# Kernel optimization log

Measured on AMD Instinct MI355X. Metric: run time of the kernel, lower is better.

The kernel has to match this reference:

```python
import jax, jax.numpy as jnp
import numpy as np

N_EMBD = 1024
N_HEAD = 16
HEAD_SIZE = N_EMBD // N_HEAD
BLOCK_SIZE = 2048
B, T = 2, 2048
EPS = 1e-5


def _layernorm(x, g, b):
    mu = jnp.mean(x, axis=-1, keepdims=True)
    var = jnp.mean(jnp.square(x - mu), axis=-1, keepdims=True)
    return (x - mu) * jax.lax.rsqrt(var + EPS) * g + b


def setup_inputs() -> dict:
    key = jax.random.key(0)
    ks = jax.random.split(key, 12)
    s = 0.02
    x = jax.random.normal(ks[0], (B, T, N_EMBD), dtype=jnp.float32)
    wq = jax.random.normal(ks[1], (N_HEAD, N_EMBD, HEAD_SIZE), jnp.float32) * s
    wk = jax.random.normal(ks[2], (N_HEAD, N_EMBD, HEAD_SIZE), jnp.float32) * s
    wv = jax.random.normal(ks[3], (N_HEAD, N_EMBD, HEAD_SIZE), jnp.float32) * s
    w_proj = jax.random.normal(ks[4], (N_EMBD, N_EMBD), jnp.float32) * s
    b_proj = jnp.zeros((N_EMBD,), jnp.float32)
    w1 = jax.random.normal(ks[5], (N_EMBD, 4 * N_EMBD), jnp.float32) * s
    b1 = jnp.zeros((4 * N_EMBD,), jnp.float32)
    w2 = jax.random.normal(ks[6], (4 * N_EMBD, N_EMBD), jnp.float32) * s
    b2 = jnp.zeros((N_EMBD,), jnp.float32)
    g1 = jnp.ones((N_EMBD,), jnp.float32)
    be1 = jnp.zeros((N_EMBD,), jnp.float32)
    g2 = jnp.ones((N_EMBD,), jnp.float32)
    be2 = jnp.zeros((N_EMBD,), jnp.float32)
    return dict(x=x, wq=wq, wk=wk, wv=wv, w_proj=w_proj, b_proj=b_proj,
                w1=w1, b1=b1, w2=w2, b2=b2, g1=g1, be1=be1, g2=g2, be2=be2)


def reference(x, wq, wk, wv, w_proj, b_proj, w1, b1, w2, b2, g1, be1, g2, be2):
    # --- self-attention with pre-LN ---
    h = _layernorm(x, g1, be1)
    q = jnp.einsum('btc,hcd->bhtd', h, wq)
    k = jnp.einsum('btc,hcd->bhtd', h, wk)
    v = jnp.einsum('btc,hcd->bhtd', h, wv)
    scores = jnp.einsum('bhtd,bhsd->bhts', q, k) / np.sqrt(HEAD_SIZE).astype(np.float32)
    causal = jnp.tril(jnp.ones((T, T), dtype=bool))
    scores = jnp.where(causal, scores, -jnp.inf)
    weights = jax.nn.softmax(scores, axis=-1)
    attn = jnp.einsum('bhts,bhsd->bhtd', weights, v)  # (B,H,T,D)
    attn = attn.transpose(0, 2, 1, 3).reshape(B, T, N_EMBD)  # concat heads
    sa = attn @ w_proj + b_proj
    x = x + sa
    # --- feed-forward with pre-LN ---
    h2 = _layernorm(x, g2, be2)
    ff = jax.nn.relu(h2 @ w1 + b1) @ w2 + b2
    return x + ff
```

## Files before the change

### kernel.cpp

```cpp
#include <hip/hip_runtime.h>
#include <hip/hip_bf16.h>
#include <cstdint>


typedef unsigned short u16;
typedef unsigned int u32;
typedef __attribute__((ext_vector_type(8))) __bf16 bf16x8;
typedef __attribute__((ext_vector_type(4))) float f32x4;

__device__ __forceinline__ u16 f2b(float f) {
    return __builtin_bit_cast(unsigned short, __float2bfloat16(f));
}

__device__ __forceinline__ f32x4 mfma16(bf16x8 a, bf16x8 b, f32x4 c) {
    return __builtin_amdgcn_mfma_f32_16x16x32_bf16(a, b, c, 0, 0, 0);
}

__device__ __forceinline__ void load_lds16(const u16* g, u16* l) {
    __builtin_amdgcn_global_load_lds(
        (const __attribute__((address_space(1))) unsigned int*)g,
        (__attribute__((address_space(3))) unsigned int*)l, 16, 0, 0);
}

__global__ __launch_bounds__(256) void transpose_all(
    const float* __restrict__ wq, const float* __restrict__ wk,
    const float* __restrict__ wv, const float* __restrict__ wp,
    const float* __restrict__ w1, const float* __restrict__ w2,
    u16* __restrict__ wqkvt, u16* __restrict__ wpt,
    u16* __restrict__ w1t, u16* __restrict__ w2t)
{
    __shared__ float tile[32][33];
    int id = blockIdx.x;
    const float* src; u16* dst; int R, C, bx, by;
    if (id < 3072) {
        const int m = id >> 10;
        src = (m == 0) ? wq : (m == 1) ? wk : wv;
        dst = wqkvt + m * 1048576u;
        int t = id & 1023;
        const int b = t >> 6; t &= 63;
        R = 1024; C = 64; bx = t & 1; by = t >> 1;
        src += (size_t)b * 65536; dst += (size_t)b * 65536;
    } else if (id < 4096) {
        int t = id - 3072; src = wp; dst = wpt;
        R = 1024; C = 1024; bx = t & 31; by = t >> 5;
    } else if (id < 8192) {
        int t = id - 4096; src = w1; dst = w1t;
        R = 1024; C = 4096; bx = t & 127; by = t >> 7;
    } else {
        int t = id - 8192; src = w2; dst = w2t;
        R = 4096; C = 1024; bx = t & 31; by = t >> 5;
    }
    const int tx = threadIdx.x, ty = threadIdx.y;
    const int c0 = bx * 32, r0 = by * 32;
#pragma unroll
    for (int i = 0; i < 4; ++i) {
        int r = ty * 4 + i;
        tile[r][tx] = src[(size_t)(r0 + r) * C + c0 + tx];
    }
    __syncthreads();
#pragma unroll
    for (int i = 0; i < 4; ++i) {
        int r = ty * 4 + i;
        dst[(size_t)(c0 + r) * R + r0 + tx] = f2b(tile[tx][r]);
    }
}

__global__ __launch_bounds__(256) void ln_kernel(
    const float* __restrict__ x, const float* __restrict__ g,
    const float* __restrict__ be, u16* __restrict__ out)
{
    const int row = blockIdx.x;
    const int tid = threadIdx.x;
    const float* xr = x + (size_t)row * 1024;
    float v[4];
#pragma unroll
    for (int i = 0; i < 4; ++i) v[i] = xr[tid + i * 256];
    float s = v[0] + v[1] + v[2] + v[3];
    float q = v[0]*v[0] + v[1]*v[1] + v[2]*v[2] + v[3]*v[3];
#pragma unroll
    for (int o = 1; o < 64; o <<= 1) {
        s += __shfl_xor(s, o, 64);
        q += __shfl_xor(q, o, 64);
    }
    __shared__ float red[8];
    const int wave = tid >> 6;
    if ((tid & 63) == 0) { red[wave] = s; red[4 + wave] = q; }
    __syncthreads();
    s = red[0] + red[1] + red[2] + red[3];
    q = red[4] + red[5] + red[6] + red[7];
    const float mu = s * (1.0f / 1024.0f);
    const float var = q * (1.0f / 1024.0f) - mu * mu;
    const float rstd = rsqrtf(var + 1e-5f);
#pragma unroll
    for (int i = 0; i < 4; ++i) {
        int idx = tid + i * 256;
        out[(size_t)row * 1024 + idx] = f2b((v[i] - mu) * rstd * g[idx] + be[idx]);
    }
}

template <int EPI, int TM, int TN, int WM, int WN, int BK>
__global__ __launch_bounds__(256, 2) void gemm_bt(
    const u16* __restrict__ A, const u16* __restrict__ Bt,
    int M, int N, int K,
    const float* __restrict__ bias, const float* __restrict__ resid_f,
    u16* __restrict__ out_b, float* __restrict__ out_f)
{
    constexpr int MI = WM / 16, NI = WN / 16;
    constexpr int MWAVES = TM / WM;
    constexpr int SS = BK / 64;
    __shared__ alignas(16) u16 As[TM * BK];
    __shared__ alignas(16) u16 Bs[TN * BK];
    const int tid = threadIdx.x;
    const int wave = tid >> 6, lane = tid & 63;
    const int lr = lane >> 4, lc = lane & 15;
    const int m0 = blockIdx.x * TM, n0 = blockIdx.y * TN;
    const int wm = (wave % MWAVES) * WM, wn = (wave / MWAVES) * WN;

    f32x4 acc[MI][NI];
#pragma unroll
    for (int i = 0; i < MI; ++i)
#pragma unroll
        for (int j = 0; j < NI; ++j) acc[i][j] = (f32x4){0.f, 0.f, 0.f, 0.f};

    const int srow = lane >> 3;
    const int skb = (lane & 7) ^ srow;
    const u16* Agp = A + (size_t)(m0 + wave * 8 + srow) * K + skb * 8;
    const u16* Bgp = Bt + (size_t)(n0 + wave * 8 + srow) * K + skb * 8;
    const int ldst = wave * 512;

    for (int k0 = 0; k0 < K; k0 += BK) {
#pragma unroll
        for (int s = 0; s < SS; ++s) {
#pragma unroll
            for (int i = 0; i < TM / 32; ++i)
                load_lds16(Agp + (size_t)i * 32 * K + k0 + s * 64,
                           As + s * TM * 64 + i * 2048 + ldst);
#pragma unroll
            for (int i = 0; i < TN / 32; ++i)
                load_lds16(Bgp + (size_t)i * 32 * K + k0 + s * 64,
                           Bs + s * TN * 64 + i * 2048 + ldst);
        }
        __syncthreads();
#pragma unroll
        for (int h = 0; h < BK / 32; ++h) {
            const int ss = h >> 1, hh = h & 1;
            const int qh = ((hh * 4 + lr) ^ (lc & 7)) * 8;
            bf16x8 af[MI], bfr[NI];
#pragma unroll
            for (int i = 0; i < MI; ++i)
                af[i] = *(const bf16x8*)&As[ss * TM * 64 + (wm + i * 16 + lc) * 64 + qh];
#pragma unroll
            for (int j = 0; j < NI; ++j)
                bfr[j] = *(const bf16x8*)&Bs[ss * TN * 64 + (wn + j * 16 + lc) * 64 + qh];
#pragma unroll
            for (int i = 0; i < MI; ++i)
#pragma unroll
                for (int j = 0; j < NI; ++j)
                    acc[i][j] = mfma16(af[i], bfr[j], acc[i][j]);
        }
        __syncthreads();
    }

#pragma unroll
    for (int i = 0; i < MI; ++i) {
#pragma unroll
        for (int j = 0; j < NI; ++j) {
#pragma unroll
            for (int r = 0; r < 4; ++r) {
                const int m = m0 + wm + i * 16 + lr * 4 + r;
                const int n = n0 + wn + j * 16 + lc;
                const float v = acc[i][j][r];
                if (EPI == 0) {
                    const int group = n >> 10, nn = n & 1023;
                    const int hh = nn >> 6, dd = nn & 63;
                    const int bb = m >> 11, tt = m & 2047;
                    if (group == 0)
                        out_b[(((size_t)(bb * 16 + hh) * 2048) + tt) * 64 + dd] =
                            f2b(v * 0.18033688f);
                    else if (group == 1)
                        out_b[4194304u + (((size_t)(bb * 16 + hh) * 2048) + tt) * 64 + dd] =
                            f2b(v);
                    else
                        out_b[8388608u + (((size_t)(bb * 16 + hh) * 64) + dd) * 2048 + tt] =
                            f2b(v);
                } else if (EPI == 4) {
                    size_t idx = (size_t)m * N + n;
                    float rv = v + bias[n];
                    out_b[idx] = f2b(rv > 0.f ? rv : 0.f);
                } else {
                    size_t idx = (size_t)m * N + n;
                    out_f[idx] = resid_f[idx] + v + bias[n];
                }
            }
        }
    }
}

__global__ __launch_bounds__(256) void attn_kernel(
    const u16* __restrict__ qb, const u16* __restrict__ kb,
    const u16* __restrict__ vtb, u16* __restrict__ ob)
{
    const int id = blockIdx.x;
    const int xcd = id & 7;
    const int xq = (id >> 3) & 15;
    const int bh = (id >> 7) * 8 + xcd;
    const int b = bh >> 4, h = bh & 15;
    const int tid = threadIdx.x, wave = tid >> 6, lane = tid & 63;
    const int lr = lane >> 4, lc = lane & 15;
    const int qx = lc & 7;
    __shared__ alignas(16) u16 Ks[64 * 64];
    __shared__ alignas(16) u16 Vts[64 * 64];
    __shared__ alignas(16) u16 Ps[4][16 * 64];
    const size_t base = (size_t)bh * (2048 * 64);

    const int srow = lane >> 3;
    const int sdb = (lane & 7) ^ srow;
    const u16* kg0 = kb + base + (size_t)(wave * 16 + srow) * 64 + sdb * 8;
    const u16* vg0 = vtb + base + (size_t)(wave * 16 + srow) * 2048 + sdb * 8;
    u16* KsW = Ks + wave * 1024;
    u16* VsW = Vts + wave * 1024;
    const int q0 = (lr ^ qx) * 8;
    const int q1 = ((4 + lr) ^ qx) * 8;
    const int wsh = lr >> 1, wsub = (lr & 1) * 4;

    for (int half = 0; half < 2; ++half) {
        const int qt = half ? (31 - xq) : xq;
        const int t0 = qt * 64;
        const int trow = t0 + wave * 16 + lc;
        const bf16x8 qf0 = *(const bf16x8*)&qb[base + (size_t)trow * 64 + lr * 8];
        const bf16x8 qf1 = *(const bf16x8*)&qb[base + (size_t)trow * 64 + 32 + lr * 8];
        f32x4 O[4];
        float pls = 0.f;
#pragma unroll
        for (int j = 0; j < 4; ++j) O[j] = (f32x4){0.f, 0.f, 0.f, 0.f};

        for (int c = 0; c <= qt; ++c) {
            const int s0 = c * 64;
            load_lds16(kg0 + (size_t)s0 * 64, KsW);
            load_lds16(kg0 + (size_t)s0 * 64 + 512, KsW + 512);
            load_lds16(vg0 + s0, VsW);
            load_lds16(vg0 + s0 + 8 * 2048, VsW + 512);
            __syncthreads();

            f32x4 st[4];
#pragma unroll
            for (int j = 0; j < 4; ++j) st[j] = (f32x4){0.f, 0.f, 0.f, 0.f};
#pragma unroll
            for (int j = 0; j < 4; ++j) {
                const int row = (j * 16 + lc) * 64;
                bf16x8 k0 = *(const bf16x8*)&Ks[row + q0];
                bf16x8 k1 = *(const bf16x8*)&Ks[row + q1];
                st[j] = mfma16(k0, qf0, st[j]);
                st[j] = mfma16(k1, qf1, st[j]);
            }
#pragma unroll
            for (int j = 0; j < 4; ++j) {
                float pv[4];
#pragma unroll
                for (int r = 0; r < 4; ++r) {
                    float e = __builtin_amdgcn_exp2f(st[j][r]);
                    if (s0 + j * 16 + lr * 4 + r > trow) e = 0.f;
                    pls += e;
                    pv[r] = e;
                }
                uint2 w;
                w.x = (u32)f2b(pv[0]) | ((u32)f2b(pv[1]) << 16);
                w.y = (u32)f2b(pv[2]) | ((u32)f2b(pv[3]) << 16);
                *(uint2*)&Ps[wave][lc * 64 + (((j * 2 + wsh) ^ qx) * 8) + wsub] = w;
            }
            const bf16x8 pf0 = *(const bf16x8*)&Ps[wave][lc * 64 + q0];
            const bf16x8 pf1 = *(const bf16x8*)&Ps[wave][lc * 64 + q1];
#pragma unroll
            for (int j = 0; j < 4; ++j) {
                const int row = (j * 16 + lc) * 64;
                bf16x8 v0 = *(const bf16x8*)&Vts[row + q0];
                bf16x8 v1 = *(const bf16x8*)&Vts[row + q1];
                O[j] = mfma16(pf0, v0, O[j]);
                O[j] = mfma16(pf1, v1, O[j]);
            }
            __syncthreads();
        }

        float l = pls;
        l += __shfl_xor(l, 16, 64);
        l += __shfl_xor(l, 32, 64);
        const float linvT = 1.0f / l;
        float linv[4];
#pragma unroll
        for (int r = 0; r < 4; ++r) linv[r] = __shfl(linvT, lr * 4 + r, 64);
#pragma unroll
        for (int j = 0; j < 4; ++j)
#pragma unroll
            for (int r = 0; r < 4; ++r) {
                const int tr = t0 + wave * 16 + lr * 4 + r;
                ob[((size_t)b * 2048 + tr) * 1024 + h * 64 + j * 16 + lc] =
                    f2b(O[j][r] * linv[r]);
            }
    }
}

extern "C" void kernel_launch(void* const* d_in, const int* in_sizes, int n_in,
                              void* d_out, int out_size, void* d_ws, size_t ws_size,
                              hipStream_t stream)
{
    (void)in_sizes; (void)n_in; (void)out_size; (void)ws_size;
    const float* x   = (const float*)d_in[0];
    const float* wq  = (const float*)d_in[1];
    const float* wk  = (const float*)d_in[2];
    const float* wv  = (const float*)d_in[3];
    const float* wp  = (const float*)d_in[4];
    const float* bp  = (const float*)d_in[5];
    const float* w1  = (const float*)d_in[6];
    const float* b1  = (const float*)d_in[7];
    const float* w2  = (const float*)d_in[8];
    const float* b2  = (const float*)d_in[9];
    const float* g1  = (const float*)d_in[10];
    const float* be1 = (const float*)d_in[11];
    const float* g2  = (const float*)d_in[12];
    const float* be2 = (const float*)d_in[13];
    float* out = (float*)d_out;

    char* ws = (char*)d_ws;
    const size_t MB = 1024ull * 1024;
    u16*   h1    = (u16*)(ws + 0);
    u16*   wqkvt = (u16*)(ws + 8 * MB);
    u16*   wpt   = (u16*)(ws + 14 * MB);
    u16*   w1t   = (u16*)(ws + 16 * MB);
    u16*   w2t   = (u16*)(ws + 24 * MB);
    u16*   qkv   = (u16*)(ws + 32 * MB);
    u16*   attnb = (u16*)(ws + 56 * MB);
    u16*   ff1   = (u16*)(ws + 32 * MB);
    float* x2    = (float*)(ws + 64 * MB);
    u16*   h2    = h1;
    u16*   qb    = qkv;
    u16*   kbf   = qkv + 4194304u;
    u16*   vtb   = qkv + 8388608u;

    transpose_all<<<12288, dim3(32, 8), 0, stream>>>(
        wq, wk, wv, wp, w1, w2, wqkvt, wpt, w1t, w2t);

    ln_kernel<<<4096, 256, 0, stream>>>(x, g1, be1, h1);

    gemm_bt<0, 128, 128, 64, 64, 64><<<dim3(32, 24), 256, 0, stream>>>(
        h1, wqkvt, 4096, 3072, 1024, nullptr, nullptr, qkv, nullptr);

    attn_kernel<<<512, 256, 0, stream>>>(qb, kbf, vtb, attnb);

    gemm_bt<3, 64, 128, 32, 64, 128><<<dim3(64, 8), 256, 0, stream>>>(
        attnb, wpt, 4096, 1024, 1024, bp, x, nullptr, x2);

    ln_kernel<<<4096, 256, 0, stream>>>(x2, g2, be2, h2);

    gemm_bt<4, 128, 128, 64, 64, 64><<<dim3(32, 32), 256, 0, stream>>>(
        h2, w1t, 4096, 4096, 1024, b1, nullptr, ff1, nullptr);

    gemm_bt<5, 64, 128, 32, 64, 128><<<dim3(64, 8), 256, 0, stream>>>(
        ff1, w2t, 4096, 1024, 4096, b2, x2, nullptr, out);
}
```

Before: 319.7 us.

## Process two adjacent query tiles per block to reuse each K/V tile

```diff
diff --git a/kernel.cpp b/kernel.cpp
--- a/kernel.cpp
+++ b/kernel.cpp
@@ -202,7 +202,7 @@
 {
     const int id = blockIdx.x;
     const int xcd = id & 7;
-    const int xq = (id >> 3) & 15;
+    const int qt = 15 - ((id >> 3) & 15);
     const int bh = (id >> 7) * 8 + xcd;
     const int b = bh >> 4, h = bh & 15;
     const int tid = threadIdx.x, wave = tid >> 6, lane = tid & 63;
@@ -223,25 +223,34 @@
     const int q1 = ((4 + lr) ^ qx) * 8;
     const int wsh = lr >> 1, wsub = (lr & 1) * 4;
 
-    for (int half = 0; half < 2; ++half) {
-        const int qt = half ? (31 - xq) : xq;
-        const int t0 = qt * 64;
-        const int trow = t0 + wave * 16 + lc;
-        const bf16x8 qf0 = *(const bf16x8*)&qb[base + (size_t)trow * 64 + lr * 8];
-        const bf16x8 qf1 = *(const bf16x8*)&qb[base + (size_t)trow * 64 + 32 + lr * 8];
-        f32x4 O[4];
-        float pls = 0.f;
-#pragma unroll
-        for (int j = 0; j < 4; ++j) O[j] = (f32x4){0.f, 0.f, 0.f, 0.f};
-
-        for (int c = 0; c <= qt; ++c) {
-            const int s0 = c * 64;
-            load_lds16(kg0 + (size_t)s0 * 64, KsW);
-            load_lds16(kg0 + (size_t)s0 * 64 + 512, KsW + 512);
-            load_lds16(vg0 + s0, VsW);
-            load_lds16(vg0 + s0 + 8 * 2048, VsW + 512);
-            __syncthreads();
-
+    const int t0 = qt * 128;
+    int trow[2];
+    bf16x8 qf[2][2];
+#pragma unroll
+    for (int u = 0; u < 2; ++u) {
+        trow[u] = t0 + u * 64 + wave * 16 + lc;
+        qf[u][0] = *(const bf16x8*)&qb[base + (size_t)trow[u] * 64 + lr * 8];
+        qf[u][1] = *(const bf16x8*)&qb[base + (size_t)trow[u] * 64 + 32 + lr * 8];
+    }
+    f32x4 O[2][4];
+    float pls[2] = {0.f, 0.f};
+#pragma unroll
+    for (int u = 0; u < 2; ++u)
+#pragma unroll
+        for (int j = 0; j < 4; ++j) O[u][j] = (f32x4){0.f, 0.f, 0.f, 0.f};
+
+    const int nch = 2 * qt + 2;
+    for (int c = 0; c < nch; ++c) {
+        const int s0 = c * 64;
+        load_lds16(kg0 + (size_t)s0 * 64, KsW);
+        load_lds16(kg0 + (size_t)s0 * 64 + 512, KsW + 512);
+        load_lds16(vg0 + s0, VsW);
+        load_lds16(vg0 + s0 + 8 * 2048, VsW + 512);
+        __syncthreads();
+
+#pragma unroll
+        for (int u = 0; u < 2; ++u) {
+            if (u == 0 && s0 >= t0 + 64) continue;
             f32x4 st[4];
 #pragma unroll
             for (int j = 0; j < 4; ++j) st[j] = (f32x4){0.f, 0.f, 0.f, 0.f};
@@ -250,8 +259,8 @@
                 const int row = (j * 16 + lc) * 64;
                 bf16x8 k0 = *(const bf16x8*)&Ks[row + q0];
                 bf16x8 k1 = *(const bf16x8*)&Ks[row + q1];
-                st[j] = mfma16(k0, qf0, st[j]);
-                st[j] = mfma16(k1, qf1, st[j]);
+                st[j] = mfma16(k0, qf[u][0], st[j]);
+                st[j] = mfma16(k1, qf[u][1], st[j]);
             }
 #pragma unroll
             for (int j = 0; j < 4; ++j) {
@@ -259,8 +268,8 @@
 #pragma unroll
                 for (int r = 0; r < 4; ++r) {
                     float e = __builtin_amdgcn_exp2f(st[j][r]);
-                    if (s0 + j * 16 + lr * 4 + r > trow) e = 0.f;
-                    pls += e;
+                    if (s0 + j * 16 + lr * 4 + r > trow[u]) e = 0.f;
+                    pls[u] += e;
                     pv[r] = e;
                 }
                 uint2 w;
@@ -275,13 +284,16 @@
                 const int row = (j * 16 + lc) * 64;
                 bf16x8 v0 = *(const bf16x8*)&Vts[row + q0];
                 bf16x8 v1 = *(const bf16x8*)&Vts[row + q1];
-                O[j] = mfma16(pf0, v0, O[j]);
-                O[j] = mfma16(pf1, v1, O[j]);
-            }
-            __syncthreads();
+                O[u][j] = mfma16(pf0, v0, O[u][j]);
+                O[u][j] = mfma16(pf1, v1, O[u][j]);
+            }
         }
-
-        float l = pls;
+        __syncthreads();
+    }
+
+#pragma unroll
+    for (int u = 0; u < 2; ++u) {
+        float l = pls[u];
         l += __shfl_xor(l, 16, 64);
         l += __shfl_xor(l, 32, 64);
         const float linvT = 1.0f / l;
@@ -292,9 +304,9 @@
         for (int j = 0; j < 4; ++j)
 #pragma unroll
             for (int r = 0; r < 4; ++r) {
-                const int tr = t0 + wave * 16 + lr * 4 + r;
+                const int tr = t0 + u * 64 + wave * 16 + lr * 4 + r;
                 ob[((size_t)b * 2048 + tr) * 1024 + h * 64 + j * 16 + lc] =
-                    f2b(O[j][r] * linv[r]);
+                    f2b(O[u][j][r] * linv[r]);
             }
     }
 }
```

Measured after the change: 334.8 us. 4.7% more time.
